# Kernel optimization log

Measured on AMD Instinct MI355X. Metric: run time of the kernel, lower is better.

The kernel has to match this reference:

```python
import jax, jax.numpy as jnp
import numpy as np

# SMPL kinematic tree: parent[i] for joint i (root's parent is -1, unused)
PARENTS = [-1, 0, 0, 0, 1, 2, 3, 4, 5, 6, 7, 8, 9, 9, 9, 12, 13, 14, 16, 17, 18, 19, 20, 21]
NUM_JOINTS = 24
NUM_VERTS = 6890
BATCH = 128


def rodrigues(r):
    """r: [K,3] axis-angle -> [K,3,3] rotation (faithful to source, incl. cos(theta*pi)/sin(theta))."""
    eps = 1e-8
    theta = jnp.linalg.norm(r + eps, axis=-1, keepdims=True)  # [K,1]
    r_hat = r / theta                                          # [K,3]
    cos = jnp.cos(theta * jnp.pi)[..., None]                   # [K,1,1]
    sin = jnp.sin(theta)[..., None]                            # [K,1,1]
    rx, ry, rz = r_hat[:, 0], r_hat[:, 1], r_hat[:, 2]
    z = jnp.zeros_like(rx)
    m = jnp.stack([z, -rz, ry, rz, z, -rx, -ry, rx, z], axis=1).reshape(-1, 3, 3)
    eye = jnp.eye(3, dtype=r.dtype)
    dot = r_hat[:, :, None] * r_hat[:, None, :]                # outer product [K,3,3]
    return cos * eye + (1.0 - cos) * dot + sin * m


def setup_inputs() -> dict:
    key = jax.random.key(0)
    k1, k2, k3, k4 = jax.random.split(key, 4)
    V = jax.random.normal(k1, (BATCH, NUM_VERTS, 3), dtype=jnp.float32)
    J = jax.random.normal(k2, (BATCH, NUM_JOINTS, 3), dtype=jnp.float32)
    pose = jax.random.normal(k3, (BATCH, NUM_JOINTS, 3), dtype=jnp.float32)
    W = jax.random.uniform(k4, (BATCH, NUM_VERTS, NUM_JOINTS), dtype=jnp.float32)
    return {"V": V, "J": J, "pose": pose, "W": W}


def reference(V, J, pose, W):
    B = V.shape[0]
    M = NUM_JOINTS
    R = rodrigues(pose.reshape(-1, 3)).reshape(B, M, 3, 3)     # [B,M,3,3]
    # local translations: root uses J[0], others J[i] - J[parent[i]]
    par = np.array(PARENTS[1:])
    t = jnp.concatenate([J[:, :1], J[:, 1:] - J[:, par]], axis=1)  # [B,M,3]
    bottom = jnp.broadcast_to(jnp.array([0.0, 0.0, 0.0, 1.0], dtype=V.dtype), (B, M, 1, 4))
    A = jnp.concatenate([jnp.concatenate([R, t[..., None]], axis=-1), bottom], axis=2)  # [B,M,4,4]
    # forward kinematics along the tree (fixed 24-joint loop; parents always precede children)
    results = [A[:, 0]]
    for i in range(1, M):
        results.append(jnp.matmul(results[PARENTS[i]], A[:, i]))
    G = jnp.stack(results, axis=1)                              # [B,M,4,4]
    # subtract transformed rest-pose joint locations (the 'pack' correction)
    Jh = jnp.concatenate([J, jnp.zeros((B, M, 1), dtype=V.dtype)], axis=-1)  # [B,M,4]
    corr = jnp.einsum('bmij,bmj->bmi', G, Jh)                   # [B,M,4]
    Gc = G - jnp.concatenate([jnp.zeros((B, M, 4, 3), dtype=V.dtype), corr[..., None]], axis=-1)
    # linear blend skinning, without materializing [B,N,M,4,4]
    Tv = jnp.einsum('bnm,bmij->bnij', W, Gc)                    # [B,N,4,4]
    Vh = jnp.concatenate([V, jnp.ones((B, V.shape[1], 1), dtype=V.dtype)], axis=-1)  # [B,N,4]
    out = jnp.einsum('bnij,bnj->bni', Tv, Vh)                   # [B,N,4]
    return out[:, :, :3]
```

## Files before the change

### kernel.cpp

```cpp
#include <hip/hip_runtime.h>
#include <math.h>
#include <string.h>

#define NJ 24
#define NV 6890
#define NB 128

__constant__ int d_anc[NJ][8] = {
  {-1,-1,-1,-1,-1,-1,-1,-1},
  { 0,-1,-1,-1,-1,-1,-1,-1},
  { 0,-1,-1,-1,-1,-1,-1,-1},
  { 0,-1,-1,-1,-1,-1,-1,-1},
  { 1, 0,-1,-1,-1,-1,-1,-1},
  { 2, 0,-1,-1,-1,-1,-1,-1},
  { 3, 0,-1,-1,-1,-1,-1,-1},
  { 4, 1, 0,-1,-1,-1,-1,-1},
  { 5, 2, 0,-1,-1,-1,-1,-1},
  { 6, 3, 0,-1,-1,-1,-1,-1},
  { 7, 4, 1, 0,-1,-1,-1,-1},
  { 8, 5, 2, 0,-1,-1,-1,-1},
  { 9, 6, 3, 0,-1,-1,-1,-1},
  { 9, 6, 3, 0,-1,-1,-1,-1},
  { 9, 6, 3, 0,-1,-1,-1,-1},
  {12, 9, 6, 3, 0,-1,-1,-1},
  {13, 9, 6, 3, 0,-1,-1,-1},
  {14, 9, 6, 3, 0,-1,-1,-1},
  {16,13, 9, 6, 3, 0,-1,-1},
  {17,14, 9, 6, 3, 0,-1,-1},
  {18,16,13, 9, 6, 3, 0,-1},
  {19,17,14, 9, 6, 3, 0,-1},
  {20,18,16,13, 9, 6, 3, 0},
  {21,19,17,14, 9, 6, 3, 0}
};
__constant__ int d_par[NJ] = {-1,0,0,0,1,2,3,4,5,6,7,8,9,9,9,12,13,14,16,17,18,19,20,21};

typedef __attribute__((ext_vector_type(8))) short bf16x8;
typedef __attribute__((ext_vector_type(4))) float f32x4;

__device__ __forceinline__ short f2bf(float f) {
    unsigned int u;
    memcpy(&u, &f, 4);
    u += 0x7fffu + ((u >> 16) & 1u);
    return (short)(u >> 16);
}

#define TLSTRIDE 20

__global__ __launch_bounds__(256) void lbs_fused(const float* __restrict__ V,
                                                 const float* __restrict__ J,
                                                 const float* __restrict__ pose,
                                                 const float* __restrict__ W,
                                                 float* __restrict__ out) {
    const int b    = blockIdx.y;
    const int tid  = threadIdx.x;
    const int wave = tid >> 6;
    const int lane = tid & 63;
    const int vwave = blockIdx.x * 1024 + wave * 256;
    const int n16 = lane & 15;
    const int g   = lane >> 4;
    const bool wactive = (vwave < NV);

    __shared__ float A_lds[NJ][12];
    __shared__ float Gc_lds[NJ * 12];
    __shared__ float tl[4 * 64 * TLSTRIDE];

    float4 pfl[4], pfh[4];
    #pragma unroll
    for (int t = 0; t < 4; t++) {
        pfl[t] = make_float4(0.f, 0.f, 0.f, 0.f);
        pfh[t] = make_float4(0.f, 0.f, 0.f, 0.f);
        if (wactive && g < 3) {
            const int v  = vwave + t * 16 + n16;
            const int vc = v < NV ? v : NV - 1;
            const float4* wp = (const float4*)(W + ((size_t)b * NV + vc) * 24 + g * 8);
            pfl[t] = wp[0];
            pfh[t] = wp[1];
        }
    }

    if (tid < NJ) {
        const int i = tid;
        const float* p = pose + ((size_t)b * NJ + i) * 3;
        float rx = p[0], ry = p[1], rz = p[2];
        float ex = rx + 1e-8f, ey = ry + 1e-8f, ez = rz + 1e-8f;
        float theta = sqrtf(ex * ex + ey * ey + ez * ez);
        float inv = 1.0f / theta;
        float hx = rx * inv, hy = ry * inv, hz = rz * inv;
        float c = cosf(theta * (float)M_PI);
        float s = sinf(theta);
        float oc = 1.0f - c;
        const float* jp = J + ((size_t)b * NJ + i) * 3;
        int par = d_par[i];
        float tx, ty, tz;
        if (par < 0) {
            tx = jp[0]; ty = jp[1]; tz = jp[2];
        } else {
            const float* jq = J + ((size_t)b * NJ + par) * 3;
            tx = jp[0] - jq[0]; ty = jp[1] - jq[1]; tz = jp[2] - jq[2];
        }
        A_lds[i][0]  = c + oc * hx * hx;
        A_lds[i][1]  = oc * hx * hy - s * hz;
        A_lds[i][2]  = oc * hx * hz + s * hy;
        A_lds[i][3]  = tx;
        A_lds[i][4]  = oc * hy * hx + s * hz;
        A_lds[i][5]  = c + oc * hy * hy;
        A_lds[i][6]  = oc * hy * hz - s * hx;
        A_lds[i][7]  = ty;
        A_lds[i][8]  = oc * hz * hx - s * hy;
        A_lds[i][9]  = oc * hz * hy + s * hx;
        A_lds[i][10] = c + oc * hz * hz;
        A_lds[i][11] = tz;
    }
    __syncthreads();

    if (tid < NJ) {
        const int i = tid;
        float M[12];
        #pragma unroll
        for (int j = 0; j < 12; j++) M[j] = A_lds[i][j];

        for (int k = 0; k < 8; k++) {
            int p = d_anc[i][k];
            if (p < 0) break;
            float P[12];
            #pragma unroll
            for (int j = 0; j < 12; j++) P[j] = A_lds[p][j];
            float N[12];
            #pragma unroll
            for (int r = 0; r < 3; r++) {
                float p0 = P[r*4+0], p1 = P[r*4+1], p2 = P[r*4+2], p3 = P[r*4+3];
                N[r*4+0] = p0 * M[0] + p1 * M[4] + p2 * M[8];
                N[r*4+1] = p0 * M[1] + p1 * M[5] + p2 * M[9];
                N[r*4+2] = p0 * M[2] + p1 * M[6] + p2 * M[10];
                N[r*4+3] = p0 * M[3] + p1 * M[7] + p2 * M[11] + p3;
            }
            #pragma unroll
            for (int j = 0; j < 12; j++) M[j] = N[j];
        }

        const float* jp = J + ((size_t)b * NJ + i) * 3;
        float jx = jp[0], jy = jp[1], jz = jp[2];
        #pragma unroll
        for (int r = 0; r < 3; r++) {
            float g0 = M[r*4+0], g1 = M[r*4+1], g2 = M[r*4+2], g3 = M[r*4+3];
            float corr = g0 * jx + g1 * jy + g2 * jz;
            Gc_lds[i*12 + r*4+0] = g0;
            Gc_lds[i*12 + r*4+1] = g1;
            Gc_lds[i*12 + r*4+2] = g2;
            Gc_lds[i*12 + r*4+3] = g3 - corr;
        }
    }
    __syncthreads();

    if (!wactive) return;

    float* mytl = &tl[wave * 64 * TLSTRIDE];

    bf16x8 bfrag;
    #pragma unroll
    for (int j = 0; j < 8; j++) {
        const int k = 8 * g + j;
        const float gval = (k < NJ && n16 < 12) ? Gc_lds[k * 12 + n16] : 0.0f;
        bfrag[j] = f2bf(gval);
    }

    auto do_tile = [&](int t, float4 l4, float4 h4) {
        bf16x8 afrag;
        afrag[0] = f2bf(l4.x); afrag[1] = f2bf(l4.y);
        afrag[2] = f2bf(l4.z); afrag[3] = f2bf(l4.w);
        afrag[4] = f2bf(h4.x); afrag[5] = f2bf(h4.y);
        afrag[6] = f2bf(h4.z); afrag[7] = f2bf(h4.w);
        f32x4 acc = {0.f, 0.f, 0.f, 0.f};
        acc = __builtin_amdgcn_mfma_f32_16x16x32_bf16(afrag, bfrag, acc, 0, 0, 0);
        #pragma unroll
        for (int r = 0; r < 4; r++) {
            const int lv = t * 16 + 4 * g + r;
            mytl[lv * TLSTRIDE + n16] = acc[r];
        }
    };

    auto do_epilogue = [&](int gbase) {
        __builtin_amdgcn_wave_barrier();
        const int gv  = gbase + lane;
        const int gvc = gv < NV ? gv : NV - 1;
        const float* row = &mytl[lane * TLSTRIDE];
        f32x4 t0 = *(const f32x4*)(row + 0);
        f32x4 t1 = *(const f32x4*)(row + 4);
        f32x4 t2 = *(const f32x4*)(row + 8);
        const float* vp = V + ((size_t)b * NV + gvc) * 3;
        const float vx = vp[0], vy = vp[1], vz = vp[2];
        if (gv < NV) {
            float* op = out + ((size_t)b * NV + gv) * 3;
            op[0] = t0[0] * vx + t0[1] * vy + t0[2] * vz + t0[3];
            op[1] = t1[0] * vx + t1[1] * vy + t1[2] * vz + t1[3];
            op[2] = t2[0] * vx + t2[1] * vy + t2[2] * vz + t2[3];
        }
        __builtin_amdgcn_wave_barrier();
    };

    #pragma unroll
    for (int t = 0; t < 4; t++) do_tile(t, pfl[t], pfh[t]);
    do_epilogue(vwave);

    #pragma unroll 1
    for (int grp = 1; grp < 4; grp++) {
        const int gbase = vwave + grp * 64;
        #pragma unroll
        for (int t = 0; t < 4; t++) {
            float4 l4 = make_float4(0.f, 0.f, 0.f, 0.f);
            float4 h4 = make_float4(0.f, 0.f, 0.f, 0.f);
            if (g < 3) {
                const int v  = gbase + t * 16 + n16;
                const int vc = v < NV ? v : NV - 1;
                const float4* wp =
                    (const float4*)(W + ((size_t)b * NV + vc) * 24 + g * 8);
                l4 = wp[0];
                h4 = wp[1];
            }
            do_tile(t, l4, h4);
        }
        do_epilogue(gbase);
    }
}

extern "C" void kernel_launch(void* const* d_in, const int* in_sizes, int n_in,
                              void* d_out, int out_size, void* d_ws, size_t ws_size,
                              hipStream_t stream) {
    const float* V    = (const float*)d_in[0];
    const float* J    = (const float*)d_in[1];
    const float* pose = (const float*)d_in[2];
    const float* W    = (const float*)d_in[3];
    float* out = (float*)d_out;

    dim3 grid((NV + 1023) / 1024, NB);
    lbs_fused<<<grid, 256, 0, stream>>>(V, J, pose, W, out);
}
```

Baseline: 24.56 us.

## Halve vertices per wave, prefetch V and next W tile before MFMA

Each wave now handles 128 vertices instead of 256, so the grid doubles (14 blocks per batch instead of 7) for more parallelism. V coordinates are loaded up front, overlapping with the joint-transform setup. The second group's W loads are issued before the first group's MFMAs and epilogue so their memory latency is hidden. launch_bounds gains a minimum-occupancy hint. The cost is that each block recomputes Rodrigues and forward kinematics twice as often in total, and register pressure rises.

```diff
diff --git a/kernel.cpp b/kernel.cpp
--- a/kernel.cpp
+++ b/kernel.cpp
@@ -46,16 +46,16 @@
 
 #define TLSTRIDE 20
 
-__global__ __launch_bounds__(256) void lbs_fused(const float* __restrict__ V,
-                                                 const float* __restrict__ J,
-                                                 const float* __restrict__ pose,
-                                                 const float* __restrict__ W,
-                                                 float* __restrict__ out) {
+__global__ __launch_bounds__(256, 4) void lbs_fused(const float* __restrict__ V,
+                                                    const float* __restrict__ J,
+                                                    const float* __restrict__ pose,
+                                                    const float* __restrict__ W,
+                                                    float* __restrict__ out) {
     const int b    = blockIdx.y;
     const int tid  = threadIdx.x;
     const int wave = tid >> 6;
     const int lane = tid & 63;
-    const int vwave = blockIdx.x * 1024 + wave * 256;
+    const int vwave = blockIdx.x * 512 + wave * 128;
     const int n16 = lane & 15;
     const int g   = lane >> 4;
     const bool wactive = (vwave < NV);
@@ -76,6 +76,17 @@
             pfl[t] = wp[0];
             pfh[t] = wp[1];
         }
+    }
+    float v0x = 0.f, v0y = 0.f, v0z = 0.f, v1x = 0.f, v1y = 0.f, v1z = 0.f;
+    if (wactive) {
+        const int e0 = vwave + lane;
+        const int e0c = e0 < NV ? e0 : NV - 1;
+        const float* vp0 = V + ((size_t)b * NV + e0c) * 3;
+        v0x = vp0[0]; v0y = vp0[1]; v0z = vp0[2];
+        const int e1 = vwave + 64 + lane;
+        const int e1c = e1 < NV ? e1 : NV - 1;
+        const float* vp1 = V + ((size_t)b * NV + e1c) * 3;
+        v1x = vp1[0]; v1y = vp1[1]; v1z = vp1[2];
     }
 
     if (tid < NJ) {
@@ -164,14 +175,16 @@
         bfrag[j] = f2bf(gval);
     }
 
-    auto do_tile = [&](int t, float4 l4, float4 h4) {
-        bf16x8 afrag;
-        afrag[0] = f2bf(l4.x); afrag[1] = f2bf(l4.y);
-        afrag[2] = f2bf(l4.z); afrag[3] = f2bf(l4.w);
-        afrag[4] = f2bf(h4.x); afrag[5] = f2bf(h4.y);
-        afrag[6] = f2bf(h4.z); afrag[7] = f2bf(h4.w);
+    auto cvt = [&](float4 l4, float4 h4) {
+        bf16x8 a;
+        a[0] = f2bf(l4.x); a[1] = f2bf(l4.y); a[2] = f2bf(l4.z); a[3] = f2bf(l4.w);
+        a[4] = f2bf(h4.x); a[5] = f2bf(h4.y); a[6] = f2bf(h4.z); a[7] = f2bf(h4.w);
+        return a;
+    };
+
+    auto mfma_store = [&](int t, bf16x8 af) {
         f32x4 acc = {0.f, 0.f, 0.f, 0.f};
-        acc = __builtin_amdgcn_mfma_f32_16x16x32_bf16(afrag, bfrag, acc, 0, 0, 0);
+        acc = __builtin_amdgcn_mfma_f32_16x16x32_bf16(af, bfrag, acc, 0, 0, 0);
         #pragma unroll
         for (int r = 0; r < 4; r++) {
             const int lv = t * 16 + 4 * g + r;
@@ -179,16 +192,13 @@
         }
     };
 
-    auto do_epilogue = [&](int gbase) {
+    auto epilogue = [&](int gbase, float vx, float vy, float vz) {
         __builtin_amdgcn_wave_barrier();
-        const int gv  = gbase + lane;
-        const int gvc = gv < NV ? gv : NV - 1;
+        const int gv = gbase + lane;
         const float* row = &mytl[lane * TLSTRIDE];
         f32x4 t0 = *(const f32x4*)(row + 0);
         f32x4 t1 = *(const f32x4*)(row + 4);
         f32x4 t2 = *(const f32x4*)(row + 8);
-        const float* vp = V + ((size_t)b * NV + gvc) * 3;
-        const float vx = vp[0], vy = vp[1], vz = vp[2];
         if (gv < NV) {
             float* op = out + ((size_t)b * NV + gv) * 3;
             op[0] = t0[0] * vx + t0[1] * vy + t0[2] * vz + t0[3];
@@ -198,29 +208,37 @@
         __builtin_amdgcn_wave_barrier();
     };
 
+    bf16x8 af0 = cvt(pfl[0], pfh[0]);
+    bf16x8 af1 = cvt(pfl[1], pfh[1]);
+    bf16x8 af2 = cvt(pfl[2], pfh[2]);
+    bf16x8 af3 = cvt(pfl[3], pfh[3]);
+
     #pragma unroll
-    for (int t = 0; t < 4; t++) do_tile(t, pfl[t], pfh[t]);
-    do_epilogue(vwave);
-
-    #pragma unroll 1
-    for (int grp = 1; grp < 4; grp++) {
-        const int gbase = vwave + grp * 64;
-        #pragma unroll
-        for (int t = 0; t < 4; t++) {
-            float4 l4 = make_float4(0.f, 0.f, 0.f, 0.f);
-            float4 h4 = make_float4(0.f, 0.f, 0.f, 0.f);
-            if (g < 3) {
-                const int v  = gbase + t * 16 + n16;
-                const int vc = v < NV ? v : NV - 1;
-                const float4* wp =
-                    (const float4*)(W + ((size_t)b * NV + vc) * 24 + g * 8);
-                l4 = wp[0];
-                h4 = wp[1];
-            }
-            do_tile(t, l4, h4);
-        }
-        do_epilogue(gbase);
-    }
+    for (int t = 0; t < 4; t++) {
+        if (g < 3) {
+            const int v  = vwave + 64 + t * 16 + n16;
+            const int vc = v < NV ? v : NV - 1;
+            const float4* wp = (const float4*)(W + ((size_t)b * NV + vc) * 24 + g * 8);
+            pfl[t] = wp[0];
+            pfh[t] = wp[1];
+        }
+    }
+
+    mfma_store(0, af0);
+    mfma_store(1, af1);
+    mfma_store(2, af2);
+    mfma_store(3, af3);
+    epilogue(vwave, v0x, v0y, v0z);
+
+    af0 = cvt(pfl[0], pfh[0]);
+    af1 = cvt(pfl[1], pfh[1]);
+    af2 = cvt(pfl[2], pfh[2]);
+    af3 = cvt(pfl[3], pfh[3]);
+    mfma_store(0, af0);
+    mfma_store(1, af1);
+    mfma_store(2, af2);
+    mfma_store(3, af3);
+    epilogue(vwave + 64, v1x, v1y, v1z);
 }
 
 extern "C" void kernel_launch(void* const* d_in, const int* in_sizes, int n_in,
@@ -232,6 +250,6 @@
     const float* W    = (const float*)d_in[3];
     float* out = (float*)d_out;
 
-    dim3 grid((NV + 1023) / 1024, NB);
+    dim3 grid((NV + 511) / 512, NB);
     lbs_fused<<<grid, 256, 0, stream>>>(V, J, pose, W, out);
 }
```

Result: slower. 25.89 us (+5.4%).
